# Kernel optimization log

Hardware: AMD Instinct MI355X
Metric: run time of the kernel (lower is better)

Reference implementation:

```python
import jax, jax.numpy as jnp
import numpy as np

B, IN, OUT, NC, S = 4096, 512, 512, 64, 1


def setup_inputs() -> dict:
    key = jax.random.key(0)
    k = jax.random.split(key, 5)
    x = jax.random.normal(k[0], (B, IN), dtype=jnp.float32)
    centers = jax.random.normal(k[1], (NC, IN), dtype=jnp.float32)
    log_sigma = jnp.zeros((NC,), dtype=jnp.float32)
    coeff_mean = jax.random.normal(k[2], (IN, OUT, NC), dtype=jnp.float32) * 0.05
    coeff_log_var = jnp.full((IN, OUT, NC), -5.0, dtype=jnp.float32)
    base_weight = jax.random.normal(k[3], (IN, OUT), dtype=jnp.float32) * 0.05
    eps = jax.random.normal(k[4], (S, IN, OUT, NC), dtype=jnp.float32)
    return {"x": x, "centers": centers, "log_sigma": log_sigma,
            "coeff_mean": coeff_mean, "coeff_log_var": coeff_log_var,
            "base_weight": base_weight, "eps": eps}


def reference(x, centers, log_sigma, coeff_mean, coeff_log_var, base_weight, eps):
    # RBF basis: (B, NC). Original repeats this along in_features, but the
    # einsum 'bin,ion->bo' with an i-constant basis equals rbf @ coeffs.sum(i).
    dist_sq = jnp.sum((x[:, None, :] - centers[None, :, :]) ** 2, axis=-1)  # (B, NC)
    sigma = jnp.exp(log_sigma)  # (NC,)
    rbf = jnp.exp(-dist_sq / (2.0 * sigma ** 2 + 1e-8))  # (B, NC)

    # Sampled variational coefficients, reparameterized.
    std = jnp.exp(0.5 * coeff_log_var)
    coeffs = coeff_mean + eps * std            # (S, IN, OUT, NC)
    c_sum = coeffs.sum(axis=1)                 # (S, OUT, NC): sum over in_features
    n_samples = eps.shape[0]
    rbf_out = jnp.einsum('bn,son->bo', rbf, c_sum) / n_samples  # mean over samples

    out = rbf_out + x @ base_weight

    # KL vs N(0, 1) prior (prior_scale = 1.0): log(var/prior_var) = coeff_log_var
    var = jnp.exp(coeff_log_var)
    kl = 0.5 * jnp.sum(var + coeff_mean ** 2 - 1.0 - coeff_log_var)
    return out, kl
```

## Files before the change

kernel.cpp:

```cpp
#include <hip/hip_runtime.h>
#include <hip/hip_bf16.h>

#define B_SZ  4096
#define IN_F  512
#define OUT_F 512
#define NC    64
#define PAIRS (OUT_F * NC)
#define TOT   (IN_F * OUT_F * NC)
#define KCH   64
#define ILEN  (IN_F / KCH)
#define KTOT  (IN_F + NC)

typedef __attribute__((ext_vector_type(8))) short bf16x8;
typedef __attribute__((ext_vector_type(4))) float f32x4;

static __device__ inline unsigned short f2bf(float f) {
    __hip_bfloat16 h = __float2bfloat16(f);
    return *(unsigned short*)&h;
}

__global__ __launch_bounds__(256)
void k1_partial_kl(const float* __restrict__ cm,
                   const float* __restrict__ clv,
                   const float* __restrict__ eps,
                   float* __restrict__ part,
                   float* __restrict__ kl_out,
                   int S) {
    int pb = blockIdx.x >> 6;
    int ch = blockIdx.x & 63;
    int p4 = pb * 1024 + threadIdx.x * 4;
    float Sf = (float)S;

    float4 s = {0.f, 0.f, 0.f, 0.f};
    float klp = 0.f;

#pragma unroll 4
    for (int ii = 0; ii < ILEN; ++ii) {
        int i = ch * ILEN + ii;
        size_t idx = (size_t)i * PAIRS + p4;
        float4 m  = *(const float4*)(cm  + idx);
        float4 lv = *(const float4*)(clv + idx);
        float4 es = *(const float4*)(eps + idx);
        for (int si = 1; si < S; ++si) {
            float4 e2 = *(const float4*)(eps + (size_t)si * TOT + idx);
            es.x += e2.x; es.y += e2.y; es.z += e2.z; es.w += e2.w;
        }
        float e1x = __expf(0.5f * lv.x);
        float e1y = __expf(0.5f * lv.y);
        float e1z = __expf(0.5f * lv.z);
        float e1w = __expf(0.5f * lv.w);
        s.x += Sf * m.x + es.x * e1x;
        s.y += Sf * m.y + es.y * e1y;
        s.z += Sf * m.z + es.z * e1z;
        s.w += Sf * m.w + es.w * e1w;
        klp += (e1x*e1x + m.x*m.x - 1.f - lv.x);
        klp += (e1y*e1y + m.y*m.y - 1.f - lv.y);
        klp += (e1z*e1z + m.z*m.z - 1.f - lv.z);
        klp += (e1w*e1w + m.w*m.w - 1.f - lv.w);
    }

    *(float4*)(part + (size_t)ch * PAIRS + p4) = s;

    for (int off = 32; off; off >>= 1)
        klp += __shfl_down(klp, off, 64);
    __shared__ float wsum[4];
    if ((threadIdx.x & 63) == 0) wsum[threadIdx.x >> 6] = klp;
    __syncthreads();
    if (threadIdx.x == 0)
        atomicAdd(kl_out, 0.5f * (wsum[0] + wsum[1] + wsum[2] + wsum[3]));
}

__global__ __launch_bounds__(256)
void k1_reduce(const float* __restrict__ part,
               unsigned short* __restrict__ wct,
               float inv_S) {
    int p4 = (blockIdx.x * 256 + threadIdx.x) * 4;
    float4 a = {0.f, 0.f, 0.f, 0.f};
#pragma unroll 8
    for (int ch = 0; ch < KCH; ++ch) {
        float4 v = *(const float4*)(part + (size_t)ch * PAIRS + p4);
        a.x += v.x; a.y += v.y; a.z += v.z; a.w += v.w;
    }
    int o = p4 >> 6, n = p4 & 63;
    ushort4 w;
    w.x = f2bf(a.x * inv_S);
    w.y = f2bf(a.y * inv_S);
    w.z = f2bf(a.z * inv_S);
    w.w = f2bf(a.w * inv_S);
    *(ushort4*)(wct + (size_t)o * KTOT + IN_F + n) = w;
}

__global__ __launch_bounds__(256)
void k_wt(const float* __restrict__ bw, unsigned short* __restrict__ wct) {
    __shared__ float tile[64 * 68];
    int bi = blockIdx.x >> 3;
    int bj = blockIdx.x & 7;
    int t = threadIdx.x;
    int cq = t & 15, rq = t >> 4;
#pragma unroll
    for (int rr = 0; rr < 4; ++rr) {
        int row = rq * 4 + rr;
        float4 v = *(const float4*)(bw + (size_t)(bi * 64 + row) * OUT_F + bj * 64 + cq * 4);
        *(float4*)&tile[row * 68 + cq * 4] = v;
    }
    __syncthreads();
#pragma unroll
    for (int rr = 0; rr < 4; ++rr) {
        int orow = rq * 4 + rr;
        ushort4 w;
        w.x = f2bf(tile[(cq * 4 + 0) * 68 + orow]);
        w.y = f2bf(tile[(cq * 4 + 1) * 68 + orow]);
        w.z = f2bf(tile[(cq * 4 + 2) * 68 + orow]);
        w.w = f2bf(tile[(cq * 4 + 3) * 68 + orow]);
        *(ushort4*)(wct + (size_t)(bj * 64 + orow) * KTOT + bi * 64 + cq * 4) = w;
    }
}

__global__ __launch_bounds__(512)
void k2_rbf(const float* __restrict__ x,
            const float* __restrict__ centers,
            const float* __restrict__ log_sigma,
            unsigned short* __restrict__ rbf) {
    __shared__ float4 xs4[2048];
    int t = threadIdx.x;
    int b0 = blockIdx.x * 16;
    int n = t >> 3, c = t & 7;

    float4 creg[16];
#pragma unroll
    for (int j = 0; j < 16; ++j)
        creg[j] = *(const float4*)(centers + (size_t)n * IN_F + c * 64 + j * 4);

    float sg  = __expf(log_sigma[n]);
    float inv = 1.f / (2.f * sg * sg + 1e-8f);

    const float4* x4 = (const float4*)(x + (size_t)b0 * IN_F);
#pragma unroll
    for (int q = 0; q < 4; ++q)
        xs4[t + q * 512] = x4[t + q * 512];
    __syncthreads();

    for (int bi = 0; bi < 16; ++bi) {
        float d = 0.f;
#pragma unroll
        for (int j = 0; j < 16; ++j) {
            float4 xv = xs4[bi * 128 + c * 16 + j];
            float dx = xv.x - creg[j].x, dy = xv.y - creg[j].y;
            float dz = xv.z - creg[j].z, dw = xv.w - creg[j].w;
            d += dx*dx + dy*dy + dz*dz + dw*dw;
        }
        d += __shfl_xor(d, 1, 64);
        d += __shfl_xor(d, 2, 64);
        d += __shfl_xor(d, 4, 64);
        if (c == 0)
            rbf[(size_t)(b0 + bi) * NC + n] = f2bf(__expf(-d * inv));
    }
}

__global__ __launch_bounds__(256)
void k3_mfma(const float* __restrict__ x,
             const unsigned short* __restrict__ rbf,
             const unsigned short* __restrict__ wct,
             float* __restrict__ out) {
    __shared__ __align__(16) unsigned short As[64 * 40];
    __shared__ __align__(16) unsigned short Bs[64 * 40];
    int t = threadIdx.x;
    int bm = blockIdx.x >> 3, bn = blockIdx.x & 7;
    int b0 = bm * 64, o0 = bn * 64;
    int r = t >> 2, ks = t & 3;
    int lane = t & 63, wv = t >> 6;
    int fm = lane & 15, kg = lane >> 4;

    f32x4 acc[4] = {{0,0,0,0},{0,0,0,0},{0,0,0,0},{0,0,0,0}};
    const int soff = r * 40 + ks * 8;
    const int aoff = (wv * 16 + fm) * 40 + kg * 8;

    for (int it = 0; it < 16; ++it) {
        int k0 = it * 32;
        float4 xa = *(const float4*)(x + (size_t)(b0 + r) * IN_F + k0 + ks * 8);
        float4 xb = *(const float4*)(x + (size_t)(b0 + r) * IN_F + k0 + ks * 8 + 4);
        ushort4 w0 = *(const ushort4*)(wct + (size_t)(o0 + r) * KTOT + k0 + ks * 8);
        ushort4 w1 = *(const ushort4*)(wct + (size_t)(o0 + r) * KTOT + k0 + ks * 8 + 4);
        __syncthreads();
        ushort4 a0 = {f2bf(xa.x), f2bf(xa.y), f2bf(xa.z), f2bf(xa.w)};
        ushort4 a1 = {f2bf(xb.x), f2bf(xb.y), f2bf(xb.z), f2bf(xb.w)};
        *(ushort4*)&As[soff]     = a0;
        *(ushort4*)&As[soff + 4] = a1;
        *(ushort4*)&Bs[soff]     = w0;
        *(ushort4*)&Bs[soff + 4] = w1;
        __syncthreads();
        bf16x8 af = *(bf16x8*)&As[aoff];
#pragma unroll
        for (int nf = 0; nf < 4; ++nf) {
            bf16x8 bfr = *(bf16x8*)&Bs[(nf * 16 + fm) * 40 + kg * 8];
            acc[nf] = __builtin_amdgcn_mfma_f32_16x16x32_bf16(af, bfr, acc[nf], 0, 0, 0);
        }
    }

    for (int it = 0; it < 2; ++it) {
        int k0 = it * 32;
        ushort4 r0 = *(const ushort4*)(rbf + (size_t)(b0 + r) * NC + k0 + ks * 8);
        ushort4 r1 = *(const ushort4*)(rbf + (size_t)(b0 + r) * NC + k0 + ks * 8 + 4);
        ushort4 w0 = *(const ushort4*)(wct + (size_t)(o0 + r) * KTOT + IN_F + k0 + ks * 8);
        ushort4 w1 = *(const ushort4*)(wct + (size_t)(o0 + r) * KTOT + IN_F + k0 + ks * 8 + 4);
        __syncthreads();
        *(ushort4*)&As[soff]     = r0;
        *(ushort4*)&As[soff + 4] = r1;
        *(ushort4*)&Bs[soff]     = w0;
        *(ushort4*)&Bs[soff + 4] = w1;
        __syncthreads();
        bf16x8 af = *(bf16x8*)&As[aoff];
#pragma unroll
        for (int nf = 0; nf < 4; ++nf) {
            bf16x8 bfr = *(bf16x8*)&Bs[(nf * 16 + fm) * 40 + kg * 8];
            acc[nf] = __builtin_amdgcn_mfma_f32_16x16x32_bf16(af, bfr, acc[nf], 0, 0, 0);
        }
    }

#pragma unroll
    for (int nf = 0; nf < 4; ++nf)
#pragma unroll
        for (int rr = 0; rr < 4; ++rr)
            out[(size_t)(b0 + wv * 16 + kg * 4 + rr) * OUT_F + o0 + nf * 16 + fm] = acc[nf][rr];
}

extern "C" void kernel_launch(void* const* d_in, const int* in_sizes, int n_in,
                              void* d_out, int out_size, void* d_ws, size_t ws_size,
                              hipStream_t stream) {
    const float* x         = (const float*)d_in[0];
    const float* centers   = (const float*)d_in[1];
    const float* log_sigma = (const float*)d_in[2];
    const float* cm        = (const float*)d_in[3];
    const float* clv       = (const float*)d_in[4];
    const float* bw        = (const float*)d_in[5];
    const float* eps       = (const float*)d_in[6];

    float* out = (float*)d_out;
    float* kl  = out + (size_t)B_SZ * OUT_F;

    float* part = (float*)d_ws;
    unsigned short* wct = (unsigned short*)(part + (size_t)KCH * PAIRS);
    unsigned short* rbf = wct + (size_t)OUT_F * KTOT;

    int S = in_sizes[6] / TOT;

    hipMemsetAsync(kl, 0, sizeof(float), stream);

    k1_partial_kl<<<2048, 256, 0, stream>>>(cm, clv, eps, part, kl, S);
    k1_reduce<<<PAIRS / 1024, 256, 0, stream>>>(part, wct, 1.0f / (float)S);
    k_wt<<<64, 256, 0, stream>>>(bw, wct);
    k2_rbf<<<B_SZ / 16, 512, 0, stream>>>(x, centers, log_sigma, rbf);
    k3_mfma<<<(B_SZ / 64) * (OUT_F / 64), 256, 0, stream>>>(x, rbf, wct, out);
}
```

Before: 275.7 us.

## Merge reduce/transpose/KL kernels, drop memset and atomics, restructure RBF distance

Collapses the partial-reduce, weight-transpose and KL finalization into one multi-role kernel and replaces the atomic KL accumulation (plus its memset) with a per-block partial array reduced deterministically. The partial kernel now uses 1024-thread blocks covering 8 rows each. The RBF kernel is reworked so each wave handles a 64-column slice of x for all centers, with an LDS cross-wave reduction, instead of staging x in shared memory. This trades fewer launches and no atomics for different memory access patterns in the streaming and RBF kernels.

```diff
diff --git a/kernel.cpp b/kernel.cpp
--- a/kernel.cpp
+++ b/kernel.cpp
@@ -5,11 +5,10 @@
 #define IN_F  512
 #define OUT_F 512
 #define NC    64
-#define PAIRS (OUT_F * NC)
-#define TOT   (IN_F * OUT_F * NC)
-#define KCH   64
-#define ILEN  (IN_F / KCH)
+#define PAIRS 32768
+#define TOT   (IN_F * PAIRS)
 #define KTOT  (IN_F + NC)
+#define RCH   64
 
 typedef __attribute__((ext_vector_type(8))) short bf16x8;
 typedef __attribute__((ext_vector_type(4))) float f32x4;
@@ -19,25 +18,23 @@
     return *(unsigned short*)&h;
 }
 
-__global__ __launch_bounds__(256)
-void k1_partial_kl(const float* __restrict__ cm,
-                   const float* __restrict__ clv,
-                   const float* __restrict__ eps,
-                   float* __restrict__ part,
-                   float* __restrict__ kl_out,
-                   int S) {
-    int pb = blockIdx.x >> 6;
-    int ch = blockIdx.x & 63;
-    int p4 = pb * 1024 + threadIdx.x * 4;
+__global__ __launch_bounds__(1024)
+void k1_partial(const float* __restrict__ cm,
+                const float* __restrict__ clv,
+                const float* __restrict__ eps,
+                float* __restrict__ part,
+                float* __restrict__ klpart,
+                int S) {
+    int pb = blockIdx.x & 7;
+    int rc = blockIdx.x >> 3;
+    int p4 = pb * 4096 + threadIdx.x * 4;
     float Sf = (float)S;
-
     float4 s = {0.f, 0.f, 0.f, 0.f};
     float klp = 0.f;
 
 #pragma unroll 4
-    for (int ii = 0; ii < ILEN; ++ii) {
-        int i = ch * ILEN + ii;
-        size_t idx = (size_t)i * PAIRS + p4;
+    for (int ii = 0; ii < 8; ++ii) {
+        size_t idx = (size_t)(rc * 8 + ii) * PAIRS + p4;
         float4 m  = *(const float4*)(cm  + idx);
         float4 lv = *(const float4*)(clv + idx);
         float4 es = *(const float4*)(eps + idx);
@@ -59,60 +56,69 @@
         klp += (e1w*e1w + m.w*m.w - 1.f - lv.w);
     }
 
-    *(float4*)(part + (size_t)ch * PAIRS + p4) = s;
+    *(float4*)(part + (size_t)rc * PAIRS + p4) = s;
 
     for (int off = 32; off; off >>= 1)
         klp += __shfl_down(klp, off, 64);
-    __shared__ float wsum[4];
+    __shared__ float wsum[16];
     if ((threadIdx.x & 63) == 0) wsum[threadIdx.x >> 6] = klp;
     __syncthreads();
-    if (threadIdx.x == 0)
-        atomicAdd(kl_out, 0.5f * (wsum[0] + wsum[1] + wsum[2] + wsum[3]));
+    if (threadIdx.x == 0) {
+        float t = 0.f;
+#pragma unroll
+        for (int i = 0; i < 16; ++i) t += wsum[i];
+        klpart[blockIdx.x] = t;
+    }
 }
 
 __global__ __launch_bounds__(256)
-void k1_reduce(const float* __restrict__ part,
-               unsigned short* __restrict__ wct,
-               float inv_S) {
-    int p4 = (blockIdx.x * 256 + threadIdx.x) * 4;
-    float4 a = {0.f, 0.f, 0.f, 0.f};
+void k_mid(const float* __restrict__ part,
+           const float* __restrict__ klpart,
+           const float* __restrict__ bw,
+           unsigned short* __restrict__ wct,
+           float* __restrict__ kl_out,
+           float inv_S) {
+    __shared__ float tile[64 * 68];
+    __shared__ float wsum[4];
+    int bid = blockIdx.x, t = threadIdx.x;
+
+    if (bid < 128) {
+        int p = bid * 256 + t;
+        float a = 0.f;
 #pragma unroll 8
-    for (int ch = 0; ch < KCH; ++ch) {
-        float4 v = *(const float4*)(part + (size_t)ch * PAIRS + p4);
-        a.x += v.x; a.y += v.y; a.z += v.z; a.w += v.w;
-    }
-    int o = p4 >> 6, n = p4 & 63;
-    ushort4 w;
-    w.x = f2bf(a.x * inv_S);
-    w.y = f2bf(a.y * inv_S);
-    w.z = f2bf(a.z * inv_S);
-    w.w = f2bf(a.w * inv_S);
-    *(ushort4*)(wct + (size_t)o * KTOT + IN_F + n) = w;
-}
-
-__global__ __launch_bounds__(256)
-void k_wt(const float* __restrict__ bw, unsigned short* __restrict__ wct) {
-    __shared__ float tile[64 * 68];
-    int bi = blockIdx.x >> 3;
-    int bj = blockIdx.x & 7;
-    int t = threadIdx.x;
-    int cq = t & 15, rq = t >> 4;
-#pragma unroll
-    for (int rr = 0; rr < 4; ++rr) {
-        int row = rq * 4 + rr;
-        float4 v = *(const float4*)(bw + (size_t)(bi * 64 + row) * OUT_F + bj * 64 + cq * 4);
-        *(float4*)&tile[row * 68 + cq * 4] = v;
-    }
-    __syncthreads();
-#pragma unroll
-    for (int rr = 0; rr < 4; ++rr) {
-        int orow = rq * 4 + rr;
-        ushort4 w;
-        w.x = f2bf(tile[(cq * 4 + 0) * 68 + orow]);
-        w.y = f2bf(tile[(cq * 4 + 1) * 68 + orow]);
-        w.z = f2bf(tile[(cq * 4 + 2) * 68 + orow]);
-        w.w = f2bf(tile[(cq * 4 + 3) * 68 + orow]);
-        *(ushort4*)(wct + (size_t)(bj * 64 + orow) * KTOT + bi * 64 + cq * 4) = w;
+        for (int r = 0; r < RCH; ++r)
+            a += part[(size_t)r * PAIRS + p];
+        int o = p >> 6, n = p & 63;
+        wct[(size_t)o * KTOT + IN_F + n] = f2bf(a * inv_S);
+    } else if (bid < 192) {
+        int bb = bid - 128;
+        int bi = bb >> 3, bj = bb & 7;
+        int cq = t & 15, rq = t >> 4;
+#pragma unroll
+        for (int rr = 0; rr < 4; ++rr) {
+            int row = rq * 4 + rr;
+            float4 v = *(const float4*)(bw + (size_t)(bi * 64 + row) * OUT_F + bj * 64 + cq * 4);
+            *(float4*)&tile[row * 68 + cq * 4] = v;
+        }
+        __syncthreads();
+#pragma unroll
+        for (int rr = 0; rr < 4; ++rr) {
+            int orow = rq * 4 + rr;
+            ushort4 w;
+            w.x = f2bf(tile[(cq * 4 + 0) * 68 + orow]);
+            w.y = f2bf(tile[(cq * 4 + 1) * 68 + orow]);
+            w.z = f2bf(tile[(cq * 4 + 2) * 68 + orow]);
+            w.w = f2bf(tile[(cq * 4 + 3) * 68 + orow]);
+            *(ushort4*)(wct + (size_t)(bj * 64 + orow) * KTOT + bi * 64 + cq * 4) = w;
+        }
+    } else {
+        float v = klpart[t] + klpart[t + 256];
+        for (int off = 32; off; off >>= 1)
+            v += __shfl_down(v, off, 64);
+        if ((t & 63) == 0) wsum[t >> 6] = v;
+        __syncthreads();
+        if (t == 0)
+            kl_out[0] = 0.5f * (wsum[0] + wsum[1] + wsum[2] + wsum[3]);
     }
 }
 
@@ -121,39 +127,52 @@
             const float* __restrict__ centers,
             const float* __restrict__ log_sigma,
             unsigned short* __restrict__ rbf) {
-    __shared__ float4 xs4[2048];
+    __shared__ float red[16][8][64];
     int t = threadIdx.x;
+    int n = t & 63;
+    int wu = __builtin_amdgcn_readfirstlane(t >> 6);
     int b0 = blockIdx.x * 16;
-    int n = t >> 3, c = t & 7;
-
-    float4 creg[16];
-#pragma unroll
-    for (int j = 0; j < 16; ++j)
-        creg[j] = *(const float4*)(centers + (size_t)n * IN_F + c * 64 + j * 4);
-
-    float sg  = __expf(log_sigma[n]);
-    float inv = 1.f / (2.f * sg * sg + 1e-8f);
-
-    const float4* x4 = (const float4*)(x + (size_t)b0 * IN_F);
-#pragma unroll
-    for (int q = 0; q < 4; ++q)
-        xs4[t + q * 512] = x4[t + q * 512];
+
+    float creg[64];
+#pragma unroll
+    for (int q = 0; q < 16; ++q) {
+        float4 v = *(const float4*)(centers + (size_t)n * IN_F + wu * 64 + q * 4);
+        creg[q * 4 + 0] = v.x; creg[q * 4 + 1] = v.y;
+        creg[q * 4 + 2] = v.z; creg[q * 4 + 3] = v.w;
+    }
+
+    float dacc[16];
+#pragma unroll
+    for (int bi = 0; bi < 16; ++bi) {
+        const float* xr = x + (size_t)(b0 + bi) * IN_F + wu * 64;
+        float d0 = 0.f, d1 = 0.f, d2 = 0.f, d3 = 0.f;
+#pragma unroll
+        for (int j = 0; j < 64; j += 4) {
+            float t0 = xr[j + 0] - creg[j + 0];
+            float t1 = xr[j + 1] - creg[j + 1];
+            float t2 = xr[j + 2] - creg[j + 2];
+            float t3 = xr[j + 3] - creg[j + 3];
+            d0 = fmaf(t0, t0, d0); d1 = fmaf(t1, t1, d1);
+            d2 = fmaf(t2, t2, d2); d3 = fmaf(t3, t3, d3);
+        }
+        dacc[bi] = (d0 + d1) + (d2 + d3);
+    }
+
+#pragma unroll
+    for (int bi = 0; bi < 16; ++bi)
+        red[bi][wu][n] = dacc[bi];
     __syncthreads();
 
-    for (int bi = 0; bi < 16; ++bi) {
-        float d = 0.f;
-#pragma unroll
-        for (int j = 0; j < 16; ++j) {
-            float4 xv = xs4[bi * 128 + c * 16 + j];
-            float dx = xv.x - creg[j].x, dy = xv.y - creg[j].y;
-            float dz = xv.z - creg[j].z, dw = xv.w - creg[j].w;
-            d += dx*dx + dy*dy + dz*dz + dw*dw;
-        }
-        d += __shfl_xor(d, 1, 64);
-        d += __shfl_xor(d, 2, 64);
-        d += __shfl_xor(d, 4, 64);
-        if (c == 0)
-            rbf[(size_t)(b0 + bi) * NC + n] = f2bf(__expf(-d * inv));
+#pragma unroll
+    for (int pass = 0; pass < 2; ++pass) {
+        int idx = pass * 512 + t;
+        int bi = idx >> 6, nn = idx & 63;
+        float s = 0.f;
+#pragma unroll
+        for (int w = 0; w < 8; ++w) s += red[bi][w][nn];
+        float sg  = __expf(log_sigma[nn]);
+        float inv = 1.f / (2.f * sg * sg + 1e-8f);
+        rbf[(size_t)(b0 + bi) * NC + nn] = f2bf(__expf(-s * inv));
     }
 }
 
@@ -238,17 +257,15 @@
     float* out = (float*)d_out;
     float* kl  = out + (size_t)B_SZ * OUT_F;
 
-    float* part = (float*)d_ws;
-    unsigned short* wct = (unsigned short*)(part + (size_t)KCH * PAIRS);
+    float* part   = (float*)d_ws;
+    float* klpart = part + (size_t)RCH * PAIRS;
+    unsigned short* wct = (unsigned short*)(klpart + 512);
     unsigned short* rbf = wct + (size_t)OUT_F * KTOT;
 
     int S = in_sizes[6] / TOT;
 
-    hipMemsetAsync(kl, 0, sizeof(float), stream);
-
-    k1_partial_kl<<<2048, 256, 0, stream>>>(cm, clv, eps, part, kl, S);
-    k1_reduce<<<PAIRS / 1024, 256, 0, stream>>>(part, wct, 1.0f / (float)S);
-    k_wt<<<64, 256, 0, stream>>>(bw, wct);
+    k1_partial<<<512, 1024, 0, stream>>>(cm, clv, eps, part, klpart, S);
+    k_mid<<<193, 256, 0, stream>>>(part, klpart, bw, wct, kl, 1.0f / (float)S);
     k2_rbf<<<B_SZ / 16, 512, 0, stream>>>(x, centers, log_sigma, rbf);
     k3_mfma<<<(B_SZ / 64) * (OUT_F / 64), 256, 0, stream>>>(x, rbf, wct, out);
 }
```

Result: faster. 264.8 us (-3.9%).
